# Optimization experiments

Hardware: AMD Instinct MI355X
Metric: run time of the kernel (lower is better)

Reference implementation:

```python
import jax, jax.numpy as jnp
import numpy as np

NEG_SLOPE = 0.2  # PyG GATConv default LeakyReLU slope
EPS = 1e-16


def gat_conv(x, edge_index, W, a_src, a_dst, bias, heads, out_ch, concat):
    """PyG-style GATConv (eval mode, add_self_loops=True).
    x: [N, F_in], edge_index: [2, E] (row0=source, row1=target).
    """
    N = x.shape[0]
    loops = jnp.arange(N, dtype=edge_index.dtype)
    src = jnp.concatenate([edge_index[0], loops])  # [E+N]
    dst = jnp.concatenate([edge_index[1], loops])

    h = (x @ W).reshape(N, heads, out_ch)            # [N, H, C]
    alpha_s = jnp.sum(h * a_src, axis=-1)            # [N, H]
    alpha_d = jnp.sum(h * a_dst, axis=-1)            # [N, H]

    e = alpha_s[src] + alpha_d[dst]                  # [E+N, H]
    e = jnp.where(e > 0, e, NEG_SLOPE * e)           # LeakyReLU

    # segment softmax over incoming edges of each target node
    m = jax.ops.segment_max(e, dst, num_segments=N)  # [N, H]
    m = jnp.where(jnp.isfinite(m), m, 0.0)
    ex = jnp.exp(e - m[dst])
    s = jax.ops.segment_sum(ex, dst, num_segments=N)  # [N, H]
    alpha = ex / (s[dst] + EPS)                       # [E+N, H]

    msg = h[src] * alpha[:, :, None]                  # [E+N, H, C]
    out = jax.ops.segment_sum(msg, dst, num_segments=N)  # [N, H, C]

    if concat:
        out = out.reshape(N, heads * out_ch)
    else:
        out = out.mean(axis=1)
    return out + bias


def setup_inputs() -> dict:
    key = jax.random.key(0)
    ks = jax.random.split(key, 10)
    N, E, F_in = 50000, 1000000, 128
    H, C, OUT = 4, 16, 40
    x = jax.random.normal(ks[0], (N, F_in), dtype=jnp.float32)
    edge_index = jax.random.randint(ks[1], (2, E), 0, N, dtype=jnp.int64)
    sc1 = 1.0 / np.sqrt(F_in)
    sc2 = 1.0 / np.sqrt(H * C)
    return {
        "x": x,
        "edge_index": edge_index,
        "W1": jax.random.normal(ks[2], (F_in, H * C), dtype=jnp.float32) * sc1,
        "a_src1": jax.random.normal(ks[3], (H, C), dtype=jnp.float32) * sc2,
        "a_dst1": jax.random.normal(ks[4], (H, C), dtype=jnp.float32) * sc2,
        "b1": jnp.zeros((H * C,), dtype=jnp.float32),
        "W2": jax.random.normal(ks[5], (H * C, OUT), dtype=jnp.float32) * sc2,
        "a_src2": jax.random.normal(ks[6], (1, OUT), dtype=jnp.float32) * 0.15,
        "a_dst2": jax.random.normal(ks[7], (1, OUT), dtype=jnp.float32) * 0.15,
        "b2": jnp.zeros((OUT,), dtype=jnp.float32),
    }


def reference(x, edge_index, W1, a_src1, a_dst1, b1, W2, a_src2, a_dst2, b2):
    h = gat_conv(x, edge_index, W1, a_src1, a_dst1, b1, heads=4, out_ch=16, concat=True)
    h = jax.nn.elu(h)  # dropout is identity in eval mode
    out = gat_conv(h, edge_index, W2, a_src2, a_dst2, b2, heads=1, out_ch=40, concat=False)
    return out
```

## Files before the change

### kernel.cpp

```cpp
#include <hip/hip_runtime.h>

#define NEG_SLOPE 0.2f
#define GAT_EPS 1e-16f
#define NB 256
#define SB 512
#define DPB 128

__device__ __forceinline__ float leaky(float e){ return e > 0.f ? e : NEG_SLOPE * e; }

__device__ __forceinline__ unsigned bf2(float a, float b){
  unsigned ua = __float_as_uint(a); ua += 0x7FFFu + ((ua >> 16) & 1u);
  unsigned ub = __float_as_uint(b); ub += 0x7FFFu + ((ub >> 16) & 1u);
  return (ua >> 16) | (ub & 0xFFFF0000u);
}
__device__ __forceinline__ float bflo(unsigned v){ return __uint_as_float(v << 16); }
__device__ __forceinline__ float bfhi(unsigned v){ return __uint_as_float(v & 0xFFFF0000u); }

__global__ __launch_bounds__(256) void k_gemm1(const float* __restrict__ x,
                                               const float* __restrict__ W,
                                               const float* __restrict__ a_src,
                                               const float* __restrict__ a_dst,
                                               unsigned* __restrict__ h1b,
                                               float* __restrict__ as1,
                                               float* __restrict__ ad1, int N){
  __shared__ float Ws[128*64];
  __shared__ float xs[64*20];
  const int t = threadIdx.x;
  const int n0 = blockIdx.x * 64;
  for (int i = t; i < 128*64/4; i += 256) ((float4*)Ws)[i] = ((const float4*)W)[i];
  const int ct = t & 15;
  const int rt = t >> 4;
  const int lr = t >> 2;
  const int lq = t & 3;
  const bool rok = (n0 + lr) < N;
  const float* xrow = x + (size_t)(n0 + lr)*128 + lq*4;
  float acc[4][4];
#pragma unroll
  for (int i = 0; i < 4; i++)
#pragma unroll
    for (int j = 0; j < 4; j++) acc[i][j] = 0.f;

  for (int kc = 0; kc < 8; kc++){
    float4 xv = {0.f,0.f,0.f,0.f};
    if (rok) xv = *(const float4*)(xrow + kc*16);
    __syncthreads();
    *(float4*)(xs + lr*20 + lq*4) = xv;
    __syncthreads();
#pragma unroll
    for (int kk = 0; kk < 16; kk++){
      const int k = kc*16 + kk;
      float4 wv = *(const float4*)(Ws + k*64 + ct*4);
      float x0 = xs[(rt*4+0)*20 + kk];
      float x1 = xs[(rt*4+1)*20 + kk];
      float x2 = xs[(rt*4+2)*20 + kk];
      float x3 = xs[(rt*4+3)*20 + kk];
      acc[0][0] += x0*wv.x; acc[0][1] += x0*wv.y; acc[0][2] += x0*wv.z; acc[0][3] += x0*wv.w;
      acc[1][0] += x1*wv.x; acc[1][1] += x1*wv.y; acc[1][2] += x1*wv.z; acc[1][3] += x1*wv.w;
      acc[2][0] += x2*wv.x; acc[2][1] += x2*wv.y; acc[2][2] += x2*wv.z; acc[2][3] += x2*wv.w;
      acc[3][0] += x3*wv.x; acc[3][1] += x3*wv.y; acc[3][2] += x3*wv.z; acc[3][3] += x3*wv.w;
    }
  }
  const int h = ct >> 2;
  const float4 asv = *(const float4*)(a_src + ct*4);
  const float4 adv = *(const float4*)(a_dst + ct*4);
#pragma unroll
  for (int i = 0; i < 4; i++){
    int n = n0 + rt*4 + i;
    float ss = acc[i][0]*asv.x + acc[i][1]*asv.y + acc[i][2]*asv.z + acc[i][3]*asv.w;
    float dd = acc[i][0]*adv.x + acc[i][1]*adv.y + acc[i][2]*adv.z + acc[i][3]*adv.w;
    ss += __shfl_xor(ss, 1); ss += __shfl_xor(ss, 2);
    dd += __shfl_xor(dd, 1); dd += __shfl_xor(dd, 2);
    if (n < N){
      h1b[(size_t)n*32 + ct*2 + 0] = bf2(acc[i][0], acc[i][1]);
      h1b[(size_t)n*32 + ct*2 + 1] = bf2(acc[i][2], acc[i][3]);
      if ((ct & 3) == 0){
        as1[(size_t)n*4 + h] = ss;
        ad1[(size_t)n*4 + h] = dd;
      }
    }
  }
}

__global__ __launch_bounds__(256) void k_cnt(const int* __restrict__ ei,
                                             int* __restrict__ bcnt,
                                             int E, int T, int nbin, int chunk){
  __shared__ int lh[SB];
  const int b = blockIdx.x;
  const int lo = b*chunk;
  const int hi = min(lo + chunk, T);
  for (int i = threadIdx.x; i < nbin; i += 256) lh[i] = 0;
  __syncthreads();
  for (int i = lo + (int)threadIdx.x; i < hi; i += 256){
    int dst = (i < E) ? ei[E+i] : (i - E);
    atomicAdd(&lh[dst >> 7], 1);
  }
  __syncthreads();
  for (int i = threadIdx.x; i < nbin; i += 256) bcnt[b*SB + i] = lh[i];
}

__global__ __launch_bounds__(512) void k_scan(const int* __restrict__ bcnt,
                                              int* __restrict__ qbase,
                                              int* __restrict__ qtot, int nbin){
  const int w = blockIdx.x*8 + ((int)threadIdx.x >> 6);
  const int l = (int)threadIdx.x & 63;
  if (w >= nbin) return;
  int vals[NB/64];
  int s = 0;
#pragma unroll
  for (int j = 0; j < NB/64; j++){
    vals[j] = bcnt[((l*(NB/64)) + j)*SB + w];
    s += vals[j];
  }
  int incl = s;
#pragma unroll
  for (int off = 1; off < 64; off <<= 1){
    int t = __shfl_up(incl, off);
    if (l >= off) incl += t;
  }
  int run = incl - s;
#pragma unroll
  for (int j = 0; j < NB/64; j++){
    qbase[((l*(NB/64)) + j)*SB + w] = run;
    run += vals[j];
  }
  if (l == 63) qtot[w] = run;
}

__global__ __launch_bounds__(256) void k_scat(const int* __restrict__ ei,
                                              const int* __restrict__ qbase,
                                              unsigned* __restrict__ queue,
                                              int E, int T, int nbin, int cap, int chunk){
  __shared__ int qb[SB];
  const int b = blockIdx.x;
  const int lo = b*chunk;
  const int hi = min(lo + chunk, T);
  for (int i = threadIdx.x; i < nbin; i += 256) qb[i] = qbase[b*SB + i];
  __syncthreads();
  for (int i = lo + (int)threadIdx.x; i < hi; i += 256){
    int src, dst;
    if (i < E){ src = ei[i]; dst = ei[E+i]; }
    else      { src = dst = i - E; }
    const int bin = dst >> 7;
    const int pos = atomicAdd(&qb[bin], 1);
    if (pos < cap)
      queue[(size_t)bin*cap + pos] = ((unsigned)dst << 16) | (unsigned)src;
  }
}

__global__ __launch_bounds__(256) void k_fillq(const int* __restrict__ qtot,
                                               const unsigned* __restrict__ queue,
                                               int* __restrict__ cnt,
                                               unsigned short* __restrict__ slots,
                                               int cap, int N){
  __shared__ int lcnt[DPB];
  const int sb = blockIdx.x;
  const int lo = sb * DPB;
  const int hi = min(lo + DPB, N);
  for (int i = threadIdx.x; i < DPB; i += 256) lcnt[i] = 0;
  __syncthreads();
  const int qn = min(qtot[sb], cap);
  const unsigned* q = queue + (size_t)sb*cap;
  for (int i = (int)threadIdx.x; i < qn; i += 256){
    const unsigned p = q[i];
    const int d = (int)(p >> 16) - lo;
    if ((unsigned)d < (unsigned)DPB){
      const int pos = atomicAdd(&lcnt[d], 1);
      if (pos < 64) slots[(size_t)(lo + d)*64 + pos] = (unsigned short)(p & 0xFFFFu);
    }
  }
  __syncthreads();
  for (int i = threadIdx.x; i < hi - lo; i += 256) cnt[lo + i] = lcnt[i];
}

__global__ __launch_bounds__(256) void k_edge1(const int* __restrict__ cnt,
     const unsigned short* __restrict__ slots, const float* __restrict__ as1,
     const float* __restrict__ ad1, const unsigned* __restrict__ h1b,
     const float* __restrict__ b1, float* __restrict__ g1, int N){
  int wave = (blockIdx.x << 2) + (threadIdx.x >> 6);
  if (wave >= N) return;
  const int lane = threadIdx.x & 63;
  const int e8 = lane >> 3;
  const int c8 = lane & 7;
  const int h  = c8 >> 1;
  const int deg = min(cnt[wave], 64);
  const int base = wave << 6;
  const float4 ad = *(const float4*)(ad1 + (size_t)wave*4);
  const float adh = (h==0)?ad.x:(h==1)?ad.y:(h==2)?ad.z:ad.w;

  float4 accA = {0.f,0.f,0.f,0.f};
  float4 accB = {0.f,0.f,0.f,0.f};
  float lsum = 0.f;
  for (int jb = 0; jb < deg; jb += 8){
    int slot = jb + e8;
    int s = 0; float p = 0.f;
    if (slot < deg){
      s = slots[base + slot];
      p = __expf(leaky(as1[(size_t)s*4 + h] + adh));
    }
    uint4 w = *(const uint4*)(h1b + (size_t)s*32 + c8*4);
    accA.x += p * bflo(w.x); accA.y += p * bfhi(w.x);
    accA.z += p * bflo(w.y); accA.w += p * bfhi(w.y);
    accB.x += p * bflo(w.z); accB.y += p * bfhi(w.z);
    accB.z += p * bflo(w.w); accB.w += p * bfhi(w.w);
    lsum += p;
  }
#pragma unroll
  for (int off = 8; off < 64; off <<= 1){
    accA.x += __shfl_xor(accA.x, off); accA.y += __shfl_xor(accA.y, off);
    accA.z += __shfl_xor(accA.z, off); accA.w += __shfl_xor(accA.w, off);
    accB.x += __shfl_xor(accB.x, off); accB.y += __shfl_xor(accB.y, off);
    accB.z += __shfl_xor(accB.z, off); accB.w += __shfl_xor(accB.w, off);
  }
  lsum += __shfl_xor(lsum, 1);
  lsum += __shfl_xor(lsum, 8);
  lsum += __shfl_xor(lsum, 16);
  lsum += __shfl_xor(lsum, 32);
  lsum *= 0.5f;

  if (e8 == 0){
    float inv = 1.f / (lsum + GAT_EPS);
    const float4 bA = *(const float4*)(b1 + c8*8);
    const float4 bB = *(const float4*)(b1 + c8*8 + 4);
    float4 vA, vB;
    vA.x = accA.x*inv + bA.x; vA.y = accA.y*inv + bA.y;
    vA.z = accA.z*inv + bA.z; vA.w = accA.w*inv + bA.w;
    vB.x = accB.x*inv + bB.x; vB.y = accB.y*inv + bB.y;
    vB.z = accB.z*inv + bB.z; vB.w = accB.w*inv + bB.w;
    vA.x = vA.x > 0.f ? vA.x : (__expf(vA.x) - 1.f);
    vA.y = vA.y > 0.f ? vA.y : (__expf(vA.y) - 1.f);
    vA.z = vA.z > 0.f ? vA.z : (__expf(vA.z) - 1.f);
    vA.w = vA.w > 0.f ? vA.w : (__expf(vA.w) - 1.f);
    vB.x = vB.x > 0.f ? vB.x : (__expf(vB.x) - 1.f);
    vB.y = vB.y > 0.f ? vB.y : (__expf(vB.y) - 1.f);
    vB.z = vB.z > 0.f ? vB.z : (__expf(vB.z) - 1.f);
    vB.w = vB.w > 0.f ? vB.w : (__expf(vB.w) - 1.f);
    *(float4*)(g1 + (size_t)wave*64 + c8*8)     = vA;
    *(float4*)(g1 + (size_t)wave*64 + c8*8 + 4) = vB;
  }
}

__global__ __launch_bounds__(256) void k_gemm2(const float* __restrict__ g1,
                                               const float* __restrict__ W2,
                                               const float* __restrict__ a_src,
                                               const float* __restrict__ a_dst,
                                               unsigned* __restrict__ h2lo,
                                               unsigned* __restrict__ h2hi,
                                               float* __restrict__ as2,
                                               float* __restrict__ ad2, int N){
  __shared__ float Ws[64*40];
  __shared__ float xs[32*64];
  const int t = threadIdx.x;
  const int n0 = blockIdx.x * 32;
  for (int i = t; i < 64*40; i += 256) Ws[i] = W2[i];
  for (int i = t; i < 32*64; i += 256){
    int n = n0 + (i >> 6);
    xs[i] = (n < N) ? g1[(size_t)n*64 + (i & 63)] : 0.f;
  }
  __syncthreads();
  const int c  = t & 63;
  const int ng = t >> 6;
  const bool act = (c < 40);
  float acc[8] = {0,0,0,0,0,0,0,0};
  if (act){
    for (int k = 0; k < 64; k++){
      float w = Ws[k*40 + c];
#pragma unroll
      for (int r = 0; r < 8; r++) acc[r] += xs[(ng*8+r)*64 + k] * w;
    }
  }
  const float av = act ? a_src[c] : 0.f;
  const float bv = act ? a_dst[c] : 0.f;
#pragma unroll
  for (int r = 0; r < 8; r++){
    int n = n0 + ng*8 + r;
    float po = __shfl_xor(acc[r], 1);
    if ((c & 1) == 0 && act && n < N){
      unsigned pk = bf2(acc[r], po);
      if (c < 32) h2lo[(size_t)n*16 + (c >> 1)] = pk;
      else        h2hi[(size_t)n*4  + ((c-32) >> 1)] = pk;
    }
    float ss = acc[r]*av, dd = acc[r]*bv;
#pragma unroll
    for (int off = 1; off < 64; off <<= 1){
      ss += __shfl_xor(ss, off);
      dd += __shfl_xor(dd, off);
    }
    if (c == 0 && n < N){ as2[n] = ss; ad2[n] = dd; }
  }
}

__global__ __launch_bounds__(256) void k_edge2(const int* __restrict__ cnt,
     const unsigned short* __restrict__ slots, const float* __restrict__ as2,
     const float* __restrict__ ad2, const unsigned* __restrict__ h2lo,
     const unsigned* __restrict__ h2hi, const float* __restrict__ b2,
     float* __restrict__ out, int N){
  int wave = (blockIdx.x << 2) + (threadIdx.x >> 6);
  if (wave >= N) return;
  const int lane = threadIdx.x & 63;
  const int e8 = lane >> 3;
  const int c8 = lane & 7;
  const int deg = min(cnt[wave], 64);
  const int base = wave << 6;
  const float adw = ad2[wave];

  float4 accA = {0.f,0.f,0.f,0.f};
  float4 accB = {0.f,0.f,0.f,0.f};
  float lsum = 0.f;
  for (int jb = 0; jb < deg; jb += 8){
    int slot = jb + e8;
    int s = 0; float p = 0.f;
    if (slot < deg){
      s = slots[base + slot];
      p = __expf(leaky(as2[s] + adw));
    }
    lsum += p;
    if (c8 < 5){
      uint4 w = (c8 < 4) ? *(const uint4*)(h2lo + (size_t)s*16 + c8*4)
                         : *(const uint4*)(h2hi + (size_t)s*4);
      accA.x += p * bflo(w.x); accA.y += p * bfhi(w.x);
      accA.z += p * bflo(w.y); accA.w += p * bfhi(w.y);
      accB.x += p * bflo(w.z); accB.y += p * bfhi(w.z);
      accB.z += p * bflo(w.w); accB.w += p * bfhi(w.w);
    }
  }
#pragma unroll
  for (int off = 8; off < 64; off <<= 1){
    accA.x += __shfl_xor(accA.x, off); accA.y += __shfl_xor(accA.y, off);
    accA.z += __shfl_xor(accA.z, off); accA.w += __shfl_xor(accA.w, off);
    accB.x += __shfl_xor(accB.x, off); accB.y += __shfl_xor(accB.y, off);
    accB.z += __shfl_xor(accB.z, off); accB.w += __shfl_xor(accB.w, off);
  }
#pragma unroll
  for (int off = 1; off < 64; off <<= 1) lsum += __shfl_xor(lsum, off);
  lsum *= 0.125f;

  if (e8 == 0 && c8 < 5){
    float inv = 1.f / (lsum + GAT_EPS);
    const float4 bA = *(const float4*)(b2 + c8*8);
    const float4 bB = *(const float4*)(b2 + c8*8 + 4);
    float4 vA, vB;
    vA.x = accA.x*inv + bA.x; vA.y = accA.y*inv + bA.y;
    vA.z = accA.z*inv + bA.z; vA.w = accA.w*inv + bA.w;
    vB.x = accB.x*inv + bB.x; vB.y = accB.y*inv + bB.y;
    vB.z = accB.z*inv + bB.z; vB.w = accB.w*inv + bB.w;
    *(float4*)(out + (size_t)wave*40 + c8*8)     = vA;
    *(float4*)(out + (size_t)wave*40 + c8*8 + 4) = vB;
  }
}

extern "C" void kernel_launch(void* const* d_in, const int* in_sizes, int n_in,
                              void* d_out, int out_size, void* d_ws, size_t ws_size,
                              hipStream_t stream){
  const float* x    = (const float*)d_in[0];
  const int*   ei   = (const int*)d_in[1];
  const float* W1   = (const float*)d_in[2];
  const float* a_s1 = (const float*)d_in[3];
  const float* a_d1 = (const float*)d_in[4];
  const float* b1   = (const float*)d_in[5];
  const float* W2   = (const float*)d_in[6];
  const float* a_s2 = (const float*)d_in[7];
  const float* a_d2 = (const float*)d_in[8];
  const float* b2   = (const float*)d_in[9];
  float* out = (float*)d_out;

  const int N = in_sizes[0] / 128;
  const int E = in_sizes[1] / 2;
  const int T = E + N;
  const int nbin = (N + DPB - 1) / DPB;
  const int chunk = (T + NB - 1) / NB;
  const int cap = ((T/nbin + 1024) + 255) & ~255;

  float* ws = (float*)d_ws;
  unsigned* h1b  = (unsigned*)ws; ws += (size_t)N*32;
  unsigned* h2lo = (unsigned*)ws; ws += (size_t)N*16;
  unsigned* h2hi = (unsigned*)ws; ws += (size_t)N*4;
  float* as1 = ws;  ws += (size_t)N*4;
  float* ad1 = ws;  ws += (size_t)N*4;
  float* g1  = ws;  ws += (size_t)N*64;
  float* as2 = ws;  ws += (size_t)N;
  float* ad2 = ws;  ws += (size_t)N;
  int* cnt   = (int*)ws;          ws += (size_t)N;
  int* bcnt  = (int*)ws;          ws += (size_t)NB*SB;
  int* qbase = (int*)ws;          ws += (size_t)NB*SB;
  int* qtot  = (int*)ws;          ws += SB;
  unsigned short* slots = (unsigned short*)ws; ws += (size_t)N*32;
  unsigned* queue = (unsigned*)ws; ws += (size_t)nbin*cap;

  hipLaunchKernelGGL(k_cnt,  dim3(NB), dim3(256), 0, stream, ei, bcnt, E, T, nbin, chunk);
  hipLaunchKernelGGL(k_scan, dim3((nbin+7)/8), dim3(512), 0, stream, bcnt, qbase, qtot, nbin);
  hipLaunchKernelGGL(k_scat, dim3(NB), dim3(256), 0, stream, ei, qbase, queue, E, T, nbin, cap, chunk);
  hipLaunchKernelGGL(k_fillq, dim3(nbin), dim3(256), 0, stream, qtot, queue, cnt, slots, cap, N);

  hipLaunchKernelGGL(k_gemm1, dim3((N+63)/64), dim3(256), 0, stream,
                     x, W1, a_s1, a_d1, h1b, as1, ad1, N);
  hipLaunchKernelGGL(k_edge1, dim3((N+3)/4), dim3(256), 0, stream,
                     cnt, slots, as1, ad1, h1b, b1, g1, N);

  hipLaunchKernelGGL(k_gemm2, dim3((N+31)/32), dim3(256), 0, stream,
                     g1, W2, a_s2, a_d2, h2lo, h2hi, as2, ad2, N);
  hipLaunchKernelGGL(k_edge2, dim3((N+3)/4), dim3(256), 0, stream,
                     cnt, slots, as2, ad2, h2lo, h2hi, b2, out, N);
}
```

Baseline: 230.2 us.

## Fuse second-layer GEMM and attention logits into first edge aggregation kernel

The layer-1 aggregation kernel now also does the layer-2 linear transform for its node. Each wave shuffles its 64 ELU outputs across lanes, multiplies them by W2, which every lane reads from global memory, and writes the bf16-packed h2 rows plus the as2/ad2 logits directly. This removes the g1 intermediate buffer, its global write and read, and one kernel launch. In exchange every wave re-reads a 40-column slice of W2 and does serial shuffle-FMA work, which adds register pressure and per-node latency.

```diff
diff --git a/kernel.cpp b/kernel.cpp
--- a/kernel.cpp
+++ b/kernel.cpp
@@ -175,7 +175,10 @@
 __global__ __launch_bounds__(256) void k_edge1(const int* __restrict__ cnt,
      const unsigned short* __restrict__ slots, const float* __restrict__ as1,
      const float* __restrict__ ad1, const unsigned* __restrict__ h1b,
-     const float* __restrict__ b1, float* __restrict__ g1, int N){
+     const float* __restrict__ b1, const float* __restrict__ W2,
+     const float* __restrict__ a_s2, const float* __restrict__ a_d2,
+     unsigned* __restrict__ h2lo, unsigned* __restrict__ h2hi,
+     float* __restrict__ as2, float* __restrict__ ad2, int N){
   int wave = (blockIdx.x << 2) + (threadIdx.x >> 6);
   if (wave >= N) return;
   const int lane = threadIdx.x & 63;
@@ -217,76 +220,60 @@
   lsum += __shfl_xor(lsum, 32);
   lsum *= 0.5f;
 
-  if (e8 == 0){
-    float inv = 1.f / (lsum + GAT_EPS);
-    const float4 bA = *(const float4*)(b1 + c8*8);
-    const float4 bB = *(const float4*)(b1 + c8*8 + 4);
-    float4 vA, vB;
-    vA.x = accA.x*inv + bA.x; vA.y = accA.y*inv + bA.y;
-    vA.z = accA.z*inv + bA.z; vA.w = accA.w*inv + bA.w;
-    vB.x = accB.x*inv + bB.x; vB.y = accB.y*inv + bB.y;
-    vB.z = accB.z*inv + bB.z; vB.w = accB.w*inv + bB.w;
-    vA.x = vA.x > 0.f ? vA.x : (__expf(vA.x) - 1.f);
-    vA.y = vA.y > 0.f ? vA.y : (__expf(vA.y) - 1.f);
-    vA.z = vA.z > 0.f ? vA.z : (__expf(vA.z) - 1.f);
-    vA.w = vA.w > 0.f ? vA.w : (__expf(vA.w) - 1.f);
-    vB.x = vB.x > 0.f ? vB.x : (__expf(vB.x) - 1.f);
-    vB.y = vB.y > 0.f ? vB.y : (__expf(vB.y) - 1.f);
-    vB.z = vB.z > 0.f ? vB.z : (__expf(vB.z) - 1.f);
-    vB.w = vB.w > 0.f ? vB.w : (__expf(vB.w) - 1.f);
-    *(float4*)(g1 + (size_t)wave*64 + c8*8)     = vA;
-    *(float4*)(g1 + (size_t)wave*64 + c8*8 + 4) = vB;
-  }
-}
-
-__global__ __launch_bounds__(256) void k_gemm2(const float* __restrict__ g1,
-                                               const float* __restrict__ W2,
-                                               const float* __restrict__ a_src,
-                                               const float* __restrict__ a_dst,
-                                               unsigned* __restrict__ h2lo,
-                                               unsigned* __restrict__ h2hi,
-                                               float* __restrict__ as2,
-                                               float* __restrict__ ad2, int N){
-  __shared__ float Ws[64*40];
-  __shared__ float xs[32*64];
-  const int t = threadIdx.x;
-  const int n0 = blockIdx.x * 32;
-  for (int i = t; i < 64*40; i += 256) Ws[i] = W2[i];
-  for (int i = t; i < 32*64; i += 256){
-    int n = n0 + (i >> 6);
-    xs[i] = (n < N) ? g1[(size_t)n*64 + (i & 63)] : 0.f;
-  }
-  __syncthreads();
-  const int c  = t & 63;
-  const int ng = t >> 6;
-  const bool act = (c < 40);
-  float acc[8] = {0,0,0,0,0,0,0,0};
-  if (act){
-    for (int k = 0; k < 64; k++){
-      float w = Ws[k*40 + c];
-#pragma unroll
-      for (int r = 0; r < 8; r++) acc[r] += xs[(ng*8+r)*64 + k] * w;
-    }
-  }
-  const float av = act ? a_src[c] : 0.f;
-  const float bv = act ? a_dst[c] : 0.f;
-#pragma unroll
-  for (int r = 0; r < 8; r++){
-    int n = n0 + ng*8 + r;
-    float po = __shfl_xor(acc[r], 1);
-    if ((c & 1) == 0 && act && n < N){
-      unsigned pk = bf2(acc[r], po);
-      if (c < 32) h2lo[(size_t)n*16 + (c >> 1)] = pk;
-      else        h2hi[(size_t)n*4  + ((c-32) >> 1)] = pk;
-    }
-    float ss = acc[r]*av, dd = acc[r]*bv;
-#pragma unroll
-    for (int off = 1; off < 64; off <<= 1){
-      ss += __shfl_xor(ss, off);
-      dd += __shfl_xor(dd, off);
-    }
-    if (c == 0 && n < N){ as2[n] = ss; ad2[n] = dd; }
-  }
+  const float inv = 1.f / (lsum + GAT_EPS);
+  const float4 bA = *(const float4*)(b1 + c8*8);
+  const float4 bB = *(const float4*)(b1 + c8*8 + 4);
+  float4 vA, vB;
+  vA.x = accA.x*inv + bA.x; vA.y = accA.y*inv + bA.y;
+  vA.z = accA.z*inv + bA.z; vA.w = accA.w*inv + bA.w;
+  vB.x = accB.x*inv + bB.x; vB.y = accB.y*inv + bB.y;
+  vB.z = accB.z*inv + bB.z; vB.w = accB.w*inv + bB.w;
+  vA.x = vA.x > 0.f ? vA.x : (__expf(vA.x) - 1.f);
+  vA.y = vA.y > 0.f ? vA.y : (__expf(vA.y) - 1.f);
+  vA.z = vA.z > 0.f ? vA.z : (__expf(vA.z) - 1.f);
+  vA.w = vA.w > 0.f ? vA.w : (__expf(vA.w) - 1.f);
+  vB.x = vB.x > 0.f ? vB.x : (__expf(vB.x) - 1.f);
+  vB.y = vB.y > 0.f ? vB.y : (__expf(vB.y) - 1.f);
+  vB.z = vB.z > 0.f ? vB.z : (__expf(vB.z) - 1.f);
+  vB.w = vB.w > 0.f ? vB.w : (__expf(vB.w) - 1.f);
+
+  const int c = lane;
+  const bool ca = (c < 40);
+  float acc2 = 0.f;
+#pragma unroll
+  for (int half = 0; half < 2; half++){
+    float w2c[32];
+#pragma unroll
+    for (int kk = 0; kk < 32; kk++)
+      w2c[kk] = ca ? W2[(half*32 + kk)*40 + c] : 0.f;
+#pragma unroll
+    for (int k8 = 0; k8 < 4; k8++){
+      const int sl = half*4 + k8;
+      acc2 += __shfl(vA.x, sl) * w2c[k8*8+0];
+      acc2 += __shfl(vA.y, sl) * w2c[k8*8+1];
+      acc2 += __shfl(vA.z, sl) * w2c[k8*8+2];
+      acc2 += __shfl(vA.w, sl) * w2c[k8*8+3];
+      acc2 += __shfl(vB.x, sl) * w2c[k8*8+4];
+      acc2 += __shfl(vB.y, sl) * w2c[k8*8+5];
+      acc2 += __shfl(vB.z, sl) * w2c[k8*8+6];
+      acc2 += __shfl(vB.w, sl) * w2c[k8*8+7];
+    }
+  }
+  const float po = __shfl_xor(acc2, 1);
+  if (ca && (c & 1) == 0){
+    unsigned pk = bf2(acc2, po);
+    if (c < 32) h2lo[(size_t)wave*16 + (c >> 1)] = pk;
+    else        h2hi[(size_t)wave*4  + ((c-32) >> 1)] = pk;
+  }
+  const float av = ca ? a_s2[c] : 0.f;
+  const float bv = ca ? a_d2[c] : 0.f;
+  float ss = acc2*av, dd = acc2*bv;
+#pragma unroll
+  for (int off = 1; off < 64; off <<= 1){
+    ss += __shfl_xor(ss, off);
+    dd += __shfl_xor(dd, off);
+  }
+  if (lane == 0){ as2[wave] = ss; ad2[wave] = dd; }
 }
 
 __global__ __launch_bounds__(256) void k_edge2(const int* __restrict__ cnt,
@@ -376,7 +363,6 @@
   unsigned* h2hi = (unsigned*)ws; ws += (size_t)N*4;
   float* as1 = ws;  ws += (size_t)N*4;
   float* ad1 = ws;  ws += (size_t)N*4;
-  float* g1  = ws;  ws += (size_t)N*64;
   float* as2 = ws;  ws += (size_t)N;
   float* ad2 = ws;  ws += (size_t)N;
   int* cnt   = (int*)ws;          ws += (size_t)N;
@@ -394,10 +380,9 @@
   hipLaunchKernelGGL(k_gemm1, dim3((N+63)/64), dim3(256), 0, stream,
                      x, W1, a_s1, a_d1, h1b, as1, ad1, N);
   hipLaunchKernelGGL(k_edge1, dim3((N+3)/4), dim3(256), 0, stream,
-                     cnt, slots, as1, ad1, h1b, b1, g1, N);
-
-  hipLaunchKernelGGL(k_gemm2, dim3((N+31)/32), dim3(256), 0, stream,
-                     g1, W2, a_s2, a_d2, h2lo, h2hi, as2, ad2, N);
+                     cnt, slots, as1, ad1, h1b, b1, W2, a_s2, a_d2,
+                     h2lo, h2hi, as2, ad2, N);
+
   hipLaunchKernelGGL(k_edge2, dim3((N+3)/4), dim3(256), 0, stream,
                      cnt, slots, as2, ad2, h2lo, h2hi, b2, out, N);
 }
```

New measurement: 265.1 us. 15.2% more time.
